# Kernel tuning notes

Hardware: AMD Instinct MI355X
Metric: run time of the kernel (lower is better)

## Reference

```python
import jax, jax.numpy as jnp
import numpy as np

B, C, H, W = 4, 96, 64, 64
N_STATE, DT_RANK, K = 16, 6, 3


def _layernorm(x, g, b, eps=1e-5):
    m = jnp.mean(x, axis=-1, keepdims=True)
    v = jnp.mean((x - m) ** 2, axis=-1, keepdims=True)
    return (x - m) / jnp.sqrt(v + eps) * g + b


def _grid_sample(img, gx, gy):
    # F.grid_sample: bilinear, align_corners=True, zeros padding; gx,gy in [-1,1], [B,Ho,Wo]
    Bc, Cc, Hi, Wi = img.shape
    fx = (gx + 1.0) * 0.5 * (Wi - 1)
    fy = (gy + 1.0) * 0.5 * (Hi - 1)
    x0 = jnp.floor(fx)
    y0 = jnp.floor(fy)
    wx1 = fx - x0
    wy1 = fy - y0

    def tap(ix, iy, w):
        valid = ((ix >= 0) & (ix < Wi) & (iy >= 0) & (iy < Hi)).astype(img.dtype)
        ic = jnp.clip(ix, 0, Wi - 1).astype(jnp.int32)
        jc = jnp.clip(iy, 0, Hi - 1).astype(jnp.int32)
        v = jax.vmap(lambda im, yy, xx: im[:, yy, xx])(img, jc, ic)  # [B,C,Ho,Wo]
        return v * (w * valid)[:, None, :, :]

    return (tap(x0, y0, (1 - wx1) * (1 - wy1)) + tap(x0 + 1, y0, wx1 * (1 - wy1))
            + tap(x0, y0 + 1, (1 - wx1) * wy1) + tap(x0 + 1, y0 + 1, wx1 * wy1))


def _resize_bilinear(img, Ho, Wo):
    # torch F.interpolate(mode='bilinear', align_corners=False)
    Bc, Cc, Hi, Wi = img.shape

    def src(n_out, n_in):
        s = jnp.maximum((jnp.arange(n_out, dtype=img.dtype) + 0.5) * (n_in / n_out) - 0.5, 0.0)
        i0 = jnp.floor(s).astype(jnp.int32)
        i1 = jnp.minimum(i0 + 1, n_in - 1)
        return i0, i1, s - i0

    y0, y1, wy = src(Ho, Hi)
    x0, x1, wx = src(Wo, Wi)
    row = img[:, :, y0, :] * (1 - wy)[None, None, :, None] + img[:, :, y1, :] * wy[None, None, :, None]
    return row[:, :, :, x0] * (1 - wx) + row[:, :, :, x1] * wx


def _conv_offset(x, conv1_w, conv1_b, ca1_w, ca1_b, ca2_w, ca2_b, ln_g, ln_b, conv2_w):
    Bc, Cc = x.shape[:2]
    p = conv1_w.shape[-1] // 2
    x1 = jax.lax.conv_general_dilated(
        x, conv1_w, (1, 1), [(p, p), (p, p)],
        dimension_numbers=("NCHW", "OIHW", "NCHW"), feature_group_count=Cc
    ) + conv1_b[None, :, None, None]
    xc = jnp.mean(x, axis=(2, 3))  # adaptive_avg_pool2d -> (1,1)
    hid = jax.nn.gelu(xc @ ca1_w.T + ca1_b, approximate=False)
    ca = jax.nn.sigmoid(hid @ ca2_w.T + ca2_b)
    x1 = x1 * ca[:, :, None, None]
    xn = _layernorm(jnp.transpose(x1, (0, 2, 3, 1)), ln_g, ln_b)
    xg = jax.nn.gelu(jnp.transpose(xn, (0, 3, 1, 2)), approximate=False)
    return jnp.einsum("bchw,oc->bohw", xg, conv2_w[:, :, 0, 0])


def _deformable(x, rpe_table, conv1_w, conv1_b, ca1_w, ca1_b, ca2_w, ca2_b, ln_g, ln_b, conv2_w):
    Bc, Cc, Hc, Wc = x.shape
    L = Hc * Wc
    off = _conv_offset(x, conv1_w, conv1_b, ca1_w, ca1_b, ca2_w, ca2_b, ln_g, ln_b, conv2_w)
    offset = off[:, :2]
    de = off[:, 2]
    rng = jnp.array([1.0 / (Hc - 1.0), 1.0 / (Wc - 1.0)], off.dtype).reshape(1, 2, 1, 1)
    offset = jnp.transpose(jnp.tanh(offset) * rng, (0, 2, 3, 1))  # [B,H,W,2] (dy,dx)
    ry = (jnp.linspace(0.5, Hc - 0.5, Hc) / (Hc - 1.0)) * 2.0 - 1.0
    rx = (jnp.linspace(0.5, Wc - 0.5, Wc) / (Wc - 1.0)) * 2.0 - 1.0
    ref = jnp.stack(jnp.meshgrid(ry, rx, indexing="ij"), -1)  # [H,W,2] (y,x)
    pos = offset + ref[None]
    de_index = jnp.tanh(de).reshape(Bc, L)
    path_ref = (jnp.linspace(0.5, L - 0.5, L) / (L - 1.0)) * 2.0 - 1.0
    path_pos = de_index + path_ref[None]
    x_sampled = _grid_sample(x, pos[..., 1], pos[..., 0])
    rpe = jnp.broadcast_to(rpe_table[None], (Bc,) + rpe_table.shape)
    rpe_bias = _resize_bilinear(rpe, Hc, Wc)
    ky = (jnp.linspace(0.0, float(Hc), Hc) / (Hc - 1.0)) * 2.0 - 1.0
    kx = (jnp.linspace(0.0, float(Wc), Wc) / (Wc - 1.0)) * 2.0 - 1.0
    key_grid = jnp.stack(jnp.meshgrid(ky, kx, indexing="ij"), -1)
    disp = (key_grid[None] - pos) * 0.5
    pos_bias = _grid_sample(rpe_bias, disp[..., 1], disp[..., 0])
    xd = (x_sampled + pos_bias).reshape(Bc, Cc, L)
    indices = jnp.argsort(path_pos, axis=-1)  # topk(k=N, largest=False) == ascending argsort
    xs2 = jnp.take_along_axis(xd, indices[:, None, :], axis=2)
    return xs2, indices


def _selective_scan(u, delta, A, Bs, Cs, Dv, delta_bias):
    Bc, KD, L = u.shape
    Kk = Bs.shape[1]
    Dd = KD // Kk
    Ns = A.shape[1]
    delta = jax.nn.softplus(delta + delta_bias[None, :, None])
    dt4 = jnp.moveaxis(delta.reshape(Bc, Kk, Dd, L), 3, 0)
    u4 = jnp.moveaxis(u.reshape(Bc, Kk, Dd, L), 3, 0)
    Bt = jnp.moveaxis(Bs, 3, 0)
    Ct = jnp.moveaxis(Cs, 3, 0)
    A3 = A.reshape(Kk, Dd, Ns)

    @jax.checkpoint
    def step(h, inp):
        dt, ut, bt, ct = inp  # [B,K,D],[B,K,D],[B,K,N],[B,K,N]
        h = jnp.exp(dt[..., None] * A3) * h + (dt * ut)[..., None] * bt[:, :, None, :]
        return h, jnp.einsum("bkdn,bkn->bkd", h, ct)

    h0 = jnp.zeros((Bc, Kk, Dd, Ns), u.dtype)
    _, ys = jax.lax.scan(step, h0, (dt4, u4, Bt, Ct))
    ys = jnp.moveaxis(ys, 0, 3).reshape(Bc, KD, L)
    return ys + u * Dv[None, :, None]


def _forward(x, x_proj_weight, dt_projs_weight, dt_projs_bias, A_logs, Ds_param,
             conv1_w, conv1_b, ca1_w, ca1_b, ca2_w, ca2_b, ln_g, ln_b, conv2_w, rpe_table):
    Bc, Dd, Hc, Wc = x.shape
    L = Hc * Wc
    Kk, _, R = dt_projs_weight.shape
    Ns = A_logs.shape[1]
    xs0 = x.reshape(Bc, Dd, L)
    xs2, indices = _deformable(x, rpe_table, conv1_w, conv1_b, ca1_w, ca1_b, ca2_w, ca2_b, ln_g, ln_b, conv2_w)
    xs = jnp.stack([xs0, xs0[..., ::-1], xs2], axis=1)  # [B,3,D,L]
    x_dbl = jnp.einsum("bkdl,kcd->bkcl", xs, x_proj_weight)
    dts, Bs, Cs = jnp.split(x_dbl, [R, R + Ns], axis=2)
    dts = jnp.einsum("bkrl,kdr->bkdl", dts, dt_projs_weight)
    A = -jnp.exp(A_logs)
    ys = _selective_scan(xs.reshape(Bc, Kk * Dd, L), dts.reshape(Bc, Kk * Dd, L),
                         A, Bs, Cs, Ds_param, dt_projs_bias.reshape(-1))
    ys = ys.reshape(Bc, Kk, Dd, L)
    inv = jnp.argsort(indices, axis=-1)  # inverse permutation (DeformableLayerReverse)
    y2 = jnp.take_along_axis(ys[:, 2], inv[:, None, :], axis=2)
    y = (ys[:, 0] + ys[:, 1][..., ::-1] + y2) / 3.0
    return jnp.transpose(y, (0, 2, 1)).reshape(Bc, Hc, Wc, Dd)


def setup_inputs():
    key = jax.random.key(0)
    ks = jax.random.split(key, 12)
    f = jnp.float32
    return {
        "x": jax.random.normal(ks[0], (B, C, H, W), f),
        "x_proj_weight": jax.random.normal(ks[1], (K, DT_RANK + 2 * N_STATE, C), f) * 0.05,
        "dt_projs_weight": jax.random.normal(ks[2], (K, C, DT_RANK), f) * 0.05,
        "dt_projs_bias": jax.random.normal(ks[3], (K, C), f) * 0.1,
        "A_logs": jnp.tile(jnp.log(jnp.arange(1, N_STATE + 1, dtype=f))[None, :], (K * C, 1)),
        "Ds_param": jnp.ones((K * C,), f),
        "conv1_w": jax.random.normal(ks[4], (C, 1, 9, 9), f) * 0.05,
        "conv1_b": jnp.zeros((C,), f),
        "ca1_w": jax.random.normal(ks[5], (C // 16, C), f) * 0.1,
        "ca1_b": jnp.zeros((C // 16,), f),
        "ca2_w": jax.random.normal(ks[6], (C, C // 16), f) * 0.1,
        "ca2_b": jnp.zeros((C,), f),
        "ln_g": jnp.ones((C,), f),
        "ln_b": jnp.zeros((C,), f),
        "conv2_w": jax.random.normal(ks[7], (3, C, 1, 1), f) * 0.05,
        "rpe_table": jax.random.normal(ks[8], (C, 7, 7), f) * 0.01,
    }


def reference(x, x_proj_weight, dt_projs_weight, dt_projs_bias, A_logs, Ds_param,
              conv1_w, conv1_b, ca1_w, ca1_b, ca2_w, ca2_b, ln_g, ln_b, conv2_w, rpe_table):
    return _forward(x, x_proj_weight, dt_projs_weight, dt_projs_bias, A_logs, Ds_param,
                    conv1_w, conv1_b, ca1_w, ca1_b, ca2_w, ca2_b, ln_g, ln_b, conv2_w, rpe_table)
```

## Files before the change

kernel.cpp:

```cpp
#include <hip/hip_runtime.h>

#define BB 4
#define CC 96
#define HH 64
#define WW 64
#define LL 4096
#define KK 3
#define RR 6
#define NN 16

__device__ __forceinline__ float geluf(float x){
    return 0.5f * x * (1.0f + erff(x * 0.70710678118654752f));
}
__device__ __forceinline__ float softplusf(float x){
    return fmaxf(x, 0.0f) + log1pf(expf(-fabsf(x)));
}
__device__ __forceinline__ float sigmoidf(float x){
    return 1.0f / (1.0f + expf(-x));
}

__global__ __launch_bounds__(256) void k_mean(const float* __restrict__ x, float* __restrict__ xc){
    int bc = blockIdx.x;
    const float* p = x + (size_t)bc * LL;
    float s = 0.f;
    for (int i = threadIdx.x; i < LL; i += 256) s += p[i];
    __shared__ float red[256];
    red[threadIdx.x] = s; __syncthreads();
    for (int st = 128; st > 0; st >>= 1){
        if (threadIdx.x < st) red[threadIdx.x] += red[threadIdx.x + st];
        __syncthreads();
    }
    if (threadIdx.x == 0) xc[bc] = red[0] * (1.0f / LL);
}

__global__ __launch_bounds__(128) void k_ca(const float* __restrict__ xc,
                     const float* __restrict__ w1, const float* __restrict__ b1,
                     const float* __restrict__ w2, const float* __restrict__ b2,
                     float* __restrict__ ca){
    int b = blockIdx.x;
    int t = threadIdx.x;
    __shared__ float hid[CC/16];
    if (t < CC/16){
        float a = b1[t];
        for (int d = 0; d < CC; d++) a += w1[t*CC + d] * xc[b*CC + d];
        hid[t] = geluf(a);
    }
    __syncthreads();
    if (t < CC){
        float a = b2[t];
        #pragma unroll
        for (int i = 0; i < CC/16; i++) a += w2[t*(CC/16) + i] * hid[i];
        ca[b*CC + t] = sigmoidf(a);
    }
}

__global__ __launch_bounds__(256) void k_conv(const float* __restrict__ x, const float* __restrict__ w,
                       const float* __restrict__ bias, const float* __restrict__ ca,
                       float* __restrict__ x1){
    int gid = blockIdx.x * 256 + threadIdx.x;
    int l = gid & (LL-1); int bc = gid >> 12;
    int c = bc % CC; int b = bc / CC;
    int h = l >> 6, wq = l & 63;
    const float* xp = x + (size_t)bc * LL;
    const float* wp = w + c * 81;
    float acc = 0.f;
    #pragma unroll
    for (int ky = 0; ky < 9; ky++){
        int yy = h + ky - 4;
        if (yy < 0 || yy >= HH) continue;
        #pragma unroll
        for (int kx = 0; kx < 9; kx++){
            int xx = wq + kx - 4;
            if (xx < 0 || xx >= WW) continue;
            acc += xp[yy*WW + xx] * wp[ky*9 + kx];
        }
    }
    x1[gid] = (acc + bias[c]) * ca[b*CC + c];
}

__global__ __launch_bounds__(256) void k_rpe(const float* __restrict__ t, float* __restrict__ out){
    int gid = blockIdx.x * 256 + threadIdx.x;
    int l = gid & (LL-1); int c = gid >> 12;
    int h = l >> 6, w = l & 63;
    float sy = fmaxf((h + 0.5f) * (7.0f/64.0f) - 0.5f, 0.f);
    float sx = fmaxf((w + 0.5f) * (7.0f/64.0f) - 0.5f, 0.f);
    int y0 = (int)floorf(sy); int x0 = (int)floorf(sx);
    float wy = sy - (float)y0, wx = sx - (float)x0;
    int y1 = min(y0 + 1, 6), x1i = min(x0 + 1, 6);
    const float* tp = t + c * 49;
    float r0 = tp[y0*7 + x0] * (1.f - wy) + tp[y1*7 + x0] * wy;
    float r1 = tp[y0*7 + x1i] * (1.f - wy) + tp[y1*7 + x1i] * wy;
    out[gid] = r0 * (1.f - wx) + r1 * wx;
}

__global__ __launch_bounds__(256) void k_off(const float* __restrict__ x1,
                      const float* __restrict__ g, const float* __restrict__ bta,
                      const float* __restrict__ w2,
                      float* __restrict__ posy, float* __restrict__ posx, float* __restrict__ path){
    int blk = blockIdx.x;
    int ltile = blk & 63; int b = blk >> 6;
    int lane = threadIdx.x & 63;
    int wg = threadIdx.x >> 6;
    int l = ltile * 64 + lane;
    const float* p = x1 + (size_t)b * CC * LL + l;
    float v[24];
    float s = 0.f, ss = 0.f;
    #pragma unroll
    for (int j = 0; j < 24; j++){
        float t = p[(size_t)(wg*24 + j) * LL];
        v[j] = t; s += t; ss += t*t;
    }
    __shared__ float ls[4][64], lss[4][64];
    ls[wg][lane] = s; lss[wg][lane] = ss;
    __syncthreads();
    s  = ls[0][lane]  + ls[1][lane]  + ls[2][lane]  + ls[3][lane];
    ss = lss[0][lane] + lss[1][lane] + lss[2][lane] + lss[3][lane];
    float m = s * (1.0f/CC);
    float rstd = rsqrtf(ss*(1.0f/CC) - m*m + 1e-5f);
    float a0 = 0.f, a1 = 0.f, a2 = 0.f;
    #pragma unroll
    for (int j = 0; j < 24; j++){
        int c = wg*24 + j;
        float xn = (v[j]-m)*rstd*g[c] + bta[c];
        float xg = geluf(xn);
        a0 = fmaf(w2[c],      xg, a0);
        a1 = fmaf(w2[CC+c],   xg, a1);
        a2 = fmaf(w2[2*CC+c], xg, a2);
    }
    __shared__ float la[3][4][64];
    la[0][wg][lane] = a0; la[1][wg][lane] = a1; la[2][wg][lane] = a2;
    __syncthreads();
    if (wg < 3){
        float a = la[wg][0][lane] + la[wg][1][lane] + la[wg][2][lane] + la[wg][3][lane];
        int h = l >> 6, w = l & 63;
        if (wg == 0)      posy[b*LL + l] = tanhf(a)*(1.0f/63.0f) + ((2*h+1)*(1.0f/63.0f) - 1.0f);
        else if (wg == 1) posx[b*LL + l] = tanhf(a)*(1.0f/63.0f) + ((2*w+1)*(1.0f/63.0f) - 1.0f);
        else              path[b*LL + l] = tanhf(a) + ((l + 0.5f)*(2.0f/4095.0f) - 1.0f);
    }
}

typedef unsigned long long u64s;
__device__ __forceinline__ u64s shflx64(u64s x, int m){
    int lo = __shfl_xor((int)(unsigned)x, m);
    int hi = __shfl_xor((int)(unsigned)(x >> 32), m);
    return ((u64s)(unsigned)hi << 32) | (unsigned)lo;
}
__device__ __forceinline__ void cex(u64s& a, u64s& b, bool up){
    u64s mn = a < b ? a : b;
    u64s mx = a < b ? b : a;
    a = up ? mn : mx;
    b = up ? mx : mn;
}
__global__ __launch_bounds__(1024) void k_sort(const float* __restrict__ path,
                                               int* __restrict__ idx, int* __restrict__ inv){
    int b = blockIdx.x;
    int t = threadIdx.x;
    __shared__ u64s lds[LL];
    u64s v[4];
    #pragma unroll
    for (int r = 0; r < 4; r++){
        int e = t*4 + r;
        unsigned u = __float_as_uint(path[b*LL + e]);
        u ^= (u >> 31) ? 0xFFFFFFFFu : 0x80000000u;
        v[r] = ((u64s)u << 32) | (unsigned)e;
    }
    for (int kk = 2; kk <= LL; kk <<= 1){
        for (int j = kk >> 1; j > 0; j >>= 1){
            if (j >= 256){
                __syncthreads();
                #pragma unroll
                for (int r = 0; r < 4; r++) lds[t*4 + r] = v[r];
                __syncthreads();
                #pragma unroll
                for (int r = 0; r < 4; r++){
                    int e = t*4 + r;
                    u64s pv = lds[e ^ j];
                    bool up    = ((e & kk) == 0);
                    bool lower = ((e & j) == 0);
                    u64s mn = v[r] < pv ? v[r] : pv;
                    u64s mx = v[r] < pv ? pv : v[r];
                    v[r] = (up == lower) ? mn : mx;
                }
            } else if (j >= 4){
                int m = j >> 2;
                #pragma unroll
                for (int r = 0; r < 4; r++){
                    u64s pv = shflx64(v[r], m);
                    bool up    = (((t*4 + r) & kk) == 0);
                    bool lower = ((t & m) == 0);
                    u64s mn = v[r] < pv ? v[r] : pv;
                    u64s mx = v[r] < pv ? pv : v[r];
                    v[r] = (up == lower) ? mn : mx;
                }
            } else if (j == 2){
                bool up = (((t*4) & kk) == 0);
                cex(v[0], v[2], up);
                cex(v[1], v[3], up);
            } else {
                if (kk == 2){
                    cex(v[0], v[1], true);
                    cex(v[2], v[3], false);
                } else {
                    bool up = (((t*4) & kk) == 0);
                    cex(v[0], v[1], up);
                    cex(v[2], v[3], up);
                }
            }
        }
    }
    #pragma unroll
    for (int r = 0; r < 4; r++){
        int e = t*4 + r;
        int id = (int)(unsigned)(v[r] & 0xFFFFFFFFu);
        idx[b*LL + e] = id;
        inv[b*LL + id] = e;
    }
}

__device__ __forceinline__ float bilin0(const float* __restrict__ img, float gx, float gy){
    float fx = (gx + 1.f) * 31.5f;
    float fy = (gy + 1.f) * 31.5f;
    float x0f = floorf(fx), y0f = floorf(fy);
    float wx = fx - x0f, wy = fy - y0f;
    int x0 = (int)x0f, y0 = (int)y0f;
    float acc = 0.f;
    bool vx0 = (x0 >= 0) & (x0 < WW), vx1 = (x0+1 >= 0) & (x0+1 < WW);
    bool vy0 = (y0 >= 0) & (y0 < HH), vy1 = (y0+1 >= 0) & (y0+1 < HH);
    if (vy0 & vx0) acc += img[y0*WW + x0]       * (1.f-wx) * (1.f-wy);
    if (vy0 & vx1) acc += img[y0*WW + x0+1]     * wx       * (1.f-wy);
    if (vy1 & vx0) acc += img[(y0+1)*WW + x0]   * (1.f-wx) * wy;
    if (vy1 & vx1) acc += img[(y0+1)*WW + x0+1] * wx       * wy;
    return acc;
}

__global__ __launch_bounds__(256) void k_sample(const float* __restrict__ x, const float* __restrict__ rpe,
                         const float* __restrict__ posy, const float* __restrict__ posx,
                         float* __restrict__ xd){
    int gid = blockIdx.x * 256 + threadIdx.x;
    int l = gid & (LL-1); int bc = gid >> 12;
    int b = bc / CC; int c = bc % CC;
    float gy = posy[b*LL + l], gx = posx[b*LL + l];
    float v = bilin0(x + (size_t)bc * LL, gx, gy);
    int h = l >> 6, w = l & 63;
    float ky = h * (128.0f/3969.0f) - 1.0f;
    float kx = w * (128.0f/3969.0f) - 1.0f;
    float v2 = bilin0(rpe + (size_t)c * LL, (kx - gx) * 0.5f, (ky - gy) * 0.5f);
    xd[gid] = v + v2;
}

__global__ __launch_bounds__(192, 1) void k_proj(const float* __restrict__ x, const float* __restrict__ xd,
    const int* __restrict__ indices, const float* __restrict__ xpw, const float* __restrict__ dtw,
    const float* __restrict__ dtb, float* __restrict__ u2, float* __restrict__ dt,
    float* __restrict__ Bst, float* __restrict__ Cst){
    int blk = blockIdx.x;
    int ltile = blk & 63; int bk = blk >> 6;
    int k = bk % KK; int b = bk / KK;
    int lane = threadIdx.x & 63;
    int w = threadIdx.x >> 6;
    const float* __restrict__ Wk = xpw + k*38*CC;
    int l = ltile * 64 + lane;
    int srcl = (k == 0) ? l : (k == 1 ? (LL-1-l) : indices[b*LL + l]);
    const float* xp = (k == 2 ? xd : x) + (size_t)b * CC * LL + srcl;

    __shared__ float vsh[CC*64];
    #pragma unroll
    for (int j = 0; j < 32; j++){
        int d = w*32 + j;
        vsh[d*64 + lane] = xp[(size_t)d * LL];
    }
    __syncthreads();

    if (w == 0){
        float acc[RR];
        #pragma unroll
        for (int i = 0; i < RR; i++) acc[i] = 0.f;
        for (int d = 0; d < CC; d++){
            float vv = vsh[d*64 + lane];
            #pragma unroll
            for (int i = 0; i < RR; i++) acc[i] = fmaf(Wk[i*CC + d], vv, acc[i]);
        }
        const float* __restrict__ Dw = dtw + k*CC*RR;
        const float* __restrict__ Db = dtb + k*CC;
        float* dtp = dt + (size_t)bk * CC * LL + l;
        #pragma unroll 8
        for (int d = 0; d < CC; d++){
            float sdt = Db[d];
            #pragma unroll
            for (int r = 0; r < RR; r++) sdt = fmaf(acc[r], Dw[d*RR + r], sdt);
            dtp[(size_t)d * LL] = softplusf(sdt);
        }
    } else if (w == 1){
        float acc[NN];
        #pragma unroll
        for (int i = 0; i < NN; i++) acc[i] = 0.f;
        for (int d = 0; d < CC; d++){
            float vv = vsh[d*64 + lane];
            #pragma unroll
            for (int i = 0; i < NN; i++) acc[i] = fmaf(Wk[(RR + i)*CC + d], vv, acc[i]);
        }
        size_t base = ((size_t)bk * LL + l) * NN;
        #pragma unroll
        for (int q = 0; q < 4; q++){
            float4 o; o.x = acc[q*4]; o.y = acc[q*4+1]; o.z = acc[q*4+2]; o.w = acc[q*4+3];
            *(float4*)(Bst + base + q*4) = o;
        }
    } else {
        float acc[NN];
        #pragma unroll
        for (int i = 0; i < NN; i++) acc[i] = 0.f;
        for (int d = 0; d < CC; d++){
            float vv = vsh[d*64 + lane];
            #pragma unroll
            for (int i = 0; i < NN; i++) acc[i] = fmaf(Wk[(RR + NN + i)*CC + d], vv, acc[i]);
        }
        size_t base = ((size_t)bk * LL + l) * NN;
        #pragma unroll
        for (int q = 0; q < 4; q++){
            float4 o; o.x = acc[q*4]; o.y = acc[q*4+1]; o.z = acc[q*4+2]; o.w = acc[q*4+3];
            *(float4*)(Cst + base + q*4) = o;
        }
        if (k == 2){
            float* up = u2 + (size_t)b * CC * LL + l;
            #pragma unroll 8
            for (int d = 0; d < CC; d++) up[(size_t)d * LL] = vsh[d*64 + lane];
        }
    }
}

#define SEG 64
#define TL 64
#define SROW 17
template<int KIND>
__device__ __forceinline__ void scan_body(int b, int d, const float* __restrict__ usrc,
    const float* __restrict__ dt, const float* __restrict__ Bst, const float* __restrict__ Cst,
    const float* __restrict__ Alog, const float* __restrict__ Ds, float* __restrict__ ys,
    float* sA, float* sB){
    int bk = b * KK + KIND;
    int tid = threadIdx.x;
    int ng = tid & 7;
    int seg = tid >> 3;
    int t0 = seg * TL;

    const float2 A2 = *(const float2*)(Alog + (KIND*CC + d)*NN + 2*ng);
    float A[2] = { -__expf(A2.x), -__expf(A2.y) };
    float Dv = Ds[KIND*CC + d];

    const float* dtp = dt + ((size_t)bk * CC + d) * LL + t0;
    const float* ub = (KIND == 1)
        ? usrc + ((size_t)b*CC + d) * LL + (LL-4-t0)
        : usrc + ((size_t)b*CC + d) * LL + t0;
    const float* Bp = Bst + ((size_t)bk * LL + t0) * NN + 2*ng;
    const float* Cp = Cst + ((size_t)bk * LL + t0) * NN + 2*ng;
    float* yp = ys + ((size_t)bk * CC + d) * LL + t0;

    float Ap[2] = {1.f,1.f}, h[2] = {0.f,0.f};
    for (int t = 0; t < TL; t += 4){
        float4 dq = *(const float4*)(dtp + t);
        float4 uq = (KIND == 1) ? *(const float4*)(ub - t) : *(const float4*)(ub + t);
        float dd[4] = {dq.x, dq.y, dq.z, dq.w};
        float uu[4];
        if (KIND == 1){ uu[0]=uq.w; uu[1]=uq.z; uu[2]=uq.y; uu[3]=uq.x; }
        else          { uu[0]=uq.x; uu[1]=uq.y; uu[2]=uq.z; uu[3]=uq.w; }
        #pragma unroll
        for (int i = 0; i < 4; i++){
            float2 Bq = *(const float2*)(Bp + (t+i)*NN);
            float du = dd[i] * uu[i];
            float a0 = __expf(dd[i] * A[0]);
            float a1 = __expf(dd[i] * A[1]);
            Ap[0] *= a0; Ap[1] *= a1;
            h[0] = fmaf(a0, h[0], du * Bq.x);
            h[1] = fmaf(a1, h[1], du * Bq.y);
        }
    }

    #pragma unroll
    for (int j = 0; j < 2; j++){
        sA[seg*SROW + 2*ng + j] = Ap[j];
        sB[seg*SROW + 2*ng + j] = h[j];
    }
    __syncthreads();
    {
        int wv = tid >> 6;
        int lane = tid & 63;
        #pragma unroll
        for (int nn = 0; nn < 2; nn++){
            int n = 2*wv + nn;
            float ca = sA[lane*SROW + n];
            float cb = sB[lane*SROW + n];
            #pragma unroll
            for (int off = 1; off < 64; off <<= 1){
                float ta = __shfl_up(ca, off);
                float tb = __shfl_up(cb, off);
                if (lane >= off){
                    cb = fmaf(ca, tb, cb);
                    ca *= ta;
                }
            }
            float cb_prev = __shfl_up(cb, 1);
            if (lane == 0) cb_prev = 0.f;
            sA[lane*SROW + n] = cb_prev;
        }
    }
    __syncthreads();
    float hc[2];
    #pragma unroll
    for (int j = 0; j < 2; j++) hc[j] = sA[seg*SROW + 2*ng + j];

    for (int t = 0; t < TL; t += 4){
        float4 dq = *(const float4*)(dtp + t);
        float4 uq = (KIND == 1) ? *(const float4*)(ub - t) : *(const float4*)(ub + t);
        float dd[4] = {dq.x, dq.y, dq.z, dq.w};
        float uu[4];
        if (KIND == 1){ uu[0]=uq.w; uu[1]=uq.z; uu[2]=uq.y; uu[3]=uq.x; }
        else          { uu[0]=uq.x; uu[1]=uq.y; uu[2]=uq.z; uu[3]=uq.w; }
        float yo[4];
        #pragma unroll
        for (int i = 0; i < 4; i++){
            float2 Bq = *(const float2*)(Bp + (t+i)*NN);
            float2 Cq = *(const float2*)(Cp + (t+i)*NN);
            float du = dd[i] * uu[i];
            float a0 = __expf(dd[i] * A[0]);
            float a1 = __expf(dd[i] * A[1]);
            hc[0] = fmaf(a0, hc[0], du * Bq.x);
            hc[1] = fmaf(a1, hc[1], du * Bq.y);
            float p = fmaf(hc[1], Cq.y, hc[0] * Cq.x);
            p += __shfl_xor(p, 1);
            p += __shfl_xor(p, 2);
            p += __shfl_xor(p, 4);
            yo[i] = fmaf(uu[i], Dv, p);
        }
        if (ng == 0){
            float4 o; o.x = yo[0]; o.y = yo[1]; o.z = yo[2]; o.w = yo[3];
            *(float4*)(yp + t) = o;
        }
    }
}

__global__ __launch_bounds__(512) void k_scan_all(const float* __restrict__ x, const float* __restrict__ u2,
    const float* __restrict__ dt, const float* __restrict__ Bst, const float* __restrict__ Cst,
    const float* __restrict__ Alog, const float* __restrict__ Ds, float* __restrict__ ys){
    __shared__ float sA[SEG*SROW];
    __shared__ float sB[SEG*SROW];
    int blk = blockIdx.x;
    int k = blk / (BB*CC);
    int r = blk % (BB*CC);
    int d = r % CC; int b = r / CC;
    if (k == 0)      scan_body<0>(b, d, x,  dt, Bst, Cst, Alog, Ds, ys, sA, sB);
    else if (k == 1) scan_body<1>(b, d, x,  dt, Bst, Cst, Alog, Ds, ys, sA, sB);
    else             scan_body<2>(b, d, u2, dt, Bst, Cst, Alog, Ds, ys, sA, sB);
}

__global__ __launch_bounds__(256) void k_comb(const float* __restrict__ ys, const int* __restrict__ inv,
                                              float* __restrict__ out){
    int tile = blockIdx.x & 63; int b = blockIdx.x >> 6;
    int l0 = tile * 64;
    __shared__ float t0[CC * 65];
    __shared__ int invs[64];
    if (threadIdx.x < 64) invs[threadIdx.x] = inv[b*LL + l0 + threadIdx.x];
    __syncthreads();
    const float* y0p = ys + (size_t)(b*KK + 0) * CC * LL;
    const float* y1p = ys + (size_t)(b*KK + 1) * CC * LL;
    const float* y2p = ys + (size_t)(b*KK + 2) * CC * LL;
    for (int it = 0; it < 24; it++){
        int e = it * 256 + threadIdx.x;
        int li = e & 63; int c = e >> 6;
        int l = l0 + li;
        float v = y0p[(size_t)c*LL + l] + y1p[(size_t)c*LL + (LL-1-l)] + y2p[(size_t)c*LL + invs[li]];
        t0[c*65 + li] = v * (1.0f/3.0f);
    }
    __syncthreads();
    for (int it = 0; it < 24; it++){
        int e = it * 256 + threadIdx.x;
        int c = e % CC; int li = e / CC;
        out[((size_t)b*LL + l0 + li) * CC + c] = t0[c*65 + li];
    }
}

extern "C" void kernel_launch(void* const* d_in, const int* in_sizes, int n_in,
                              void* d_out, int out_size, void* d_ws, size_t ws_size,
                              hipStream_t stream){
    const float* x    = (const float*)d_in[0];
    const float* xpw  = (const float*)d_in[1];
    const float* dtw  = (const float*)d_in[2];
    const float* dtb  = (const float*)d_in[3];
    const float* Alog = (const float*)d_in[4];
    const float* Ds   = (const float*)d_in[5];
    const float* c1w  = (const float*)d_in[6];
    const float* c1b  = (const float*)d_in[7];
    const float* ca1w = (const float*)d_in[8];
    const float* ca1b = (const float*)d_in[9];
    const float* ca2w = (const float*)d_in[10];
    const float* ca2b = (const float*)d_in[11];
    const float* lng  = (const float*)d_in[12];
    const float* lnb  = (const float*)d_in[13];
    const float* c2w  = (const float*)d_in[14];
    const float* rpet = (const float*)d_in[15];
    float* out = (float*)d_out;

    float* ws   = (float*)d_ws;
    float* xc   = ws;
    float* ca   = xc + 384;
    float* x1   = ca + 384;
    float* rpe  = x1 + (size_t)BB*CC*LL;
    float* posy = rpe + (size_t)CC*LL;
    float* posx = posy + (size_t)BB*LL;
    float* path = posx + (size_t)BB*LL;
    float* xd   = path + (size_t)BB*LL;
    int*   idx  = (int*)(xd + (size_t)BB*CC*LL);
    int*   inv  = idx + (size_t)BB*LL;
    float* u2   = (float*)(inv + (size_t)BB*LL);
    float* dtA  = u2 + (size_t)BB*CC*LL;
    float* Bst  = dtA + (size_t)BB*KK*CC*LL;
    float* Cst  = Bst + (size_t)BB*KK*LL*NN;
    float* ysA  = Cst + (size_t)BB*KK*LL*NN;

    k_mean  <<<BB*CC, 256, 0, stream>>>(x, xc);
    k_ca    <<<BB, 128, 0, stream>>>(xc, ca1w, ca1b, ca2w, ca2b, ca);
    k_conv  <<<(BB*CC*LL)/256, 256, 0, stream>>>(x, c1w, c1b, ca, x1);
    k_rpe   <<<(CC*LL)/256, 256, 0, stream>>>(rpet, rpe);
    k_off   <<<BB*64, 256, 0, stream>>>(x1, lng, lnb, c2w, posy, posx, path);
    k_sort  <<<BB, 1024, 0, stream>>>(path, idx, inv);
    k_sample<<<(BB*CC*LL)/256, 256, 0, stream>>>(x, rpe, posy, posx, xd);
    k_proj  <<<BB*KK*64, 192, 0, stream>>>(x, xd, idx, xpw, dtw, dtb, u2, dtA, Bst, Cst);
    k_scan_all<<<KK*BB*CC, 512, 0, stream>>>(x, u2, dtA, Bst, Cst, Alog, Ds, ysA);
    k_comb  <<<BB*64, 256, 0, stream>>>(ysA, inv, out);
}
```

Baseline: 354.1 us.

## Scan two channels per block with longer segments; load proj inputs into registers

The selective scan now puts two channels in each 512-thread block. Adjacent thread pairs handle the two channels, so each thread's B/C loads are shared across them, and segments grow to 128 timesteps with 32 segments. The inter-segment prefix now runs on 32-lane halves of each wave. Separately, k_proj drops its shared-memory staging of the 96 input values: every thread loads all 96 into registers, which removes a barrier but triples the global reads per block and raises register pressure. The longer serial segments reduce parallelism per block, and halving the grid cuts the number of blocks.

```diff
diff --git a/kernel.cpp b/kernel.cpp
--- a/kernel.cpp
+++ b/kernel.cpp
@@ -262,22 +262,18 @@
     int srcl = (k == 0) ? l : (k == 1 ? (LL-1-l) : indices[b*LL + l]);
     const float* xp = (k == 2 ? xd : x) + (size_t)b * CC * LL + srcl;
 
-    __shared__ float vsh[CC*64];
-    #pragma unroll
-    for (int j = 0; j < 32; j++){
-        int d = w*32 + j;
-        vsh[d*64 + lane] = xp[(size_t)d * LL];
-    }
-    __syncthreads();
+    float v[CC];
+    #pragma unroll
+    for (int d = 0; d < CC; d++) v[d] = xp[(size_t)d * LL];
 
     if (w == 0){
         float acc[RR];
         #pragma unroll
         for (int i = 0; i < RR; i++) acc[i] = 0.f;
+        #pragma unroll
         for (int d = 0; d < CC; d++){
-            float vv = vsh[d*64 + lane];
             #pragma unroll
-            for (int i = 0; i < RR; i++) acc[i] = fmaf(Wk[i*CC + d], vv, acc[i]);
+            for (int i = 0; i < RR; i++) acc[i] = fmaf(Wk[i*CC + d], v[d], acc[i]);
         }
         const float* __restrict__ Dw = dtw + k*CC*RR;
         const float* __restrict__ Db = dtb + k*CC;
@@ -293,10 +289,10 @@
         float acc[NN];
         #pragma unroll
         for (int i = 0; i < NN; i++) acc[i] = 0.f;
+        #pragma unroll
         for (int d = 0; d < CC; d++){
-            float vv = vsh[d*64 + lane];
             #pragma unroll
-            for (int i = 0; i < NN; i++) acc[i] = fmaf(Wk[(RR + i)*CC + d], vv, acc[i]);
+            for (int i = 0; i < NN; i++) acc[i] = fmaf(Wk[(RR + i)*CC + d], v[d], acc[i]);
         }
         size_t base = ((size_t)bk * LL + l) * NN;
         #pragma unroll
@@ -308,10 +304,10 @@
         float acc[NN];
         #pragma unroll
         for (int i = 0; i < NN; i++) acc[i] = 0.f;
+        #pragma unroll
         for (int d = 0; d < CC; d++){
-            float vv = vsh[d*64 + lane];
             #pragma unroll
-            for (int i = 0; i < NN; i++) acc[i] = fmaf(Wk[(RR + NN + i)*CC + d], vv, acc[i]);
+            for (int i = 0; i < NN; i++) acc[i] = fmaf(Wk[(RR + NN + i)*CC + d], v[d], acc[i]);
         }
         size_t base = ((size_t)bk * LL + l) * NN;
         #pragma unroll
@@ -321,24 +317,26 @@
         }
         if (k == 2){
             float* up = u2 + (size_t)b * CC * LL + l;
-            #pragma unroll 8
-            for (int d = 0; d < CC; d++) up[(size_t)d * LL] = vsh[d*64 + lane];
-        }
-    }
-}
-
-#define SEG 64
-#define TL 64
-#define SROW 17
+            #pragma unroll
+            for (int d = 0; d < CC; d++) up[(size_t)d * LL] = v[d];
+        }
+    }
+}
+
+#define SEG 32
+#define TL 128
+#define SROW 33
 template<int KIND>
-__device__ __forceinline__ void scan_body(int b, int d, const float* __restrict__ usrc,
+__device__ __forceinline__ void scan_body(int b, int dg, const float* __restrict__ usrc,
     const float* __restrict__ dt, const float* __restrict__ Bst, const float* __restrict__ Cst,
     const float* __restrict__ Alog, const float* __restrict__ Ds, float* __restrict__ ys,
     float* sA, float* sB){
     int bk = b * KK + KIND;
     int tid = threadIdx.x;
-    int ng = tid & 7;
-    int seg = tid >> 3;
+    int d_local = tid & 1;
+    int ng = (tid >> 1) & 7;
+    int seg = tid >> 4;
+    int d = dg*2 + d_local;
     int t0 = seg * TL;
 
     const float2 A2 = *(const float2*)(Alog + (KIND*CC + d)*NN + 2*ng);
@@ -375,36 +373,38 @@
 
     #pragma unroll
     for (int j = 0; j < 2; j++){
-        sA[seg*SROW + 2*ng + j] = Ap[j];
-        sB[seg*SROW + 2*ng + j] = h[j];
+        sA[seg*SROW + d_local*16 + 2*ng + j] = Ap[j];
+        sB[seg*SROW + d_local*16 + 2*ng + j] = h[j];
     }
     __syncthreads();
     {
         int wv = tid >> 6;
         int lane = tid & 63;
-        #pragma unroll
-        for (int nn = 0; nn < 2; nn++){
-            int n = 2*wv + nn;
-            float ca = sA[lane*SROW + n];
-            float cb = sB[lane*SROW + n];
+        int lane_in = lane & 31;
+        int half = lane >> 5;
+        #pragma unroll
+        for (int p = 0; p < 2; p++){
+            int col = wv*4 + p*2 + half;
+            float ca = sA[lane_in*SROW + col];
+            float cb = sB[lane_in*SROW + col];
             #pragma unroll
-            for (int off = 1; off < 64; off <<= 1){
+            for (int off = 1; off < 32; off <<= 1){
                 float ta = __shfl_up(ca, off);
                 float tb = __shfl_up(cb, off);
-                if (lane >= off){
+                if (lane_in >= off){
                     cb = fmaf(ca, tb, cb);
                     ca *= ta;
                 }
             }
             float cb_prev = __shfl_up(cb, 1);
-            if (lane == 0) cb_prev = 0.f;
-            sA[lane*SROW + n] = cb_prev;
+            if (lane_in == 0) cb_prev = 0.f;
+            sA[lane_in*SROW + col] = cb_prev;
         }
     }
     __syncthreads();
     float hc[2];
     #pragma unroll
-    for (int j = 0; j < 2; j++) hc[j] = sA[seg*SROW + 2*ng + j];
+    for (int j = 0; j < 2; j++) hc[j] = sA[seg*SROW + d_local*16 + 2*ng + j];
 
     for (int t = 0; t < TL; t += 4){
         float4 dq = *(const float4*)(dtp + t);
@@ -424,9 +424,9 @@
             hc[0] = fmaf(a0, hc[0], du * Bq.x);
             hc[1] = fmaf(a1, hc[1], du * Bq.y);
             float p = fmaf(hc[1], Cq.y, hc[0] * Cq.x);
-            p += __shfl_xor(p, 1);
             p += __shfl_xor(p, 2);
             p += __shfl_xor(p, 4);
+            p += __shfl_xor(p, 8);
             yo[i] = fmaf(uu[i], Dv, p);
         }
         if (ng == 0){
@@ -442,12 +442,12 @@
     __shared__ float sA[SEG*SROW];
     __shared__ float sB[SEG*SROW];
     int blk = blockIdx.x;
-    int k = blk / (BB*CC);
-    int r = blk % (BB*CC);
-    int d = r % CC; int b = r / CC;
-    if (k == 0)      scan_body<0>(b, d, x,  dt, Bst, Cst, Alog, Ds, ys, sA, sB);
-    else if (k == 1) scan_body<1>(b, d, x,  dt, Bst, Cst, Alog, Ds, ys, sA, sB);
-    else             scan_body<2>(b, d, u2, dt, Bst, Cst, Alog, Ds, ys, sA, sB);
+    int k = blk / (BB*(CC/2));
+    int r = blk % (BB*(CC/2));
+    int dg = r % (CC/2); int b = r / (CC/2);
+    if (k == 0)      scan_body<0>(b, dg, x,  dt, Bst, Cst, Alog, Ds, ys, sA, sB);
+    else if (k == 1) scan_body<1>(b, dg, x,  dt, Bst, Cst, Alog, Ds, ys, sA, sB);
+    else             scan_body<2>(b, dg, u2, dt, Bst, Cst, Alog, Ds, ys, sA, sB);
 }
 
 __global__ __launch_bounds__(256) void k_comb(const float* __restrict__ ys, const int* __restrict__ inv,
@@ -522,6 +522,6 @@
     k_sort  <<<BB, 1024, 0, stream>>>(path, idx, inv);
     k_sample<<<(BB*CC*LL)/256, 256, 0, stream>>>(x, rpe, posy, posx, xd);
     k_proj  <<<BB*KK*64, 192, 0, stream>>>(x, xd, idx, xpw, dtw, dtb, u2, dtA, Bst, Cst);
-    k_scan_all<<<KK*BB*CC, 512, 0, stream>>>(x, u2, dtA, Bst, Cst, Alog, Ds, ysA);
+    k_scan_all<<<KK*BB*(CC/2), 512, 0, stream>>>(x, u2, dtA, Bst, Cst, Alog, Ds, ysA);
     k_comb  <<<BB*64, 256, 0, stream>>>(ysA, inv, out);
 }
```

Measured after the change: 399.7 us. 1.13x slower.
